# Kernel tuning notes

Measured on AMD Instinct MI355X. Metric: run time of the kernel, lower is better.

Reference implementation:

```python
import jax, jax.numpy as jnp
import numpy as np

NUM_QUBITS = 12
ENC_COPIES = 1
ANSATZ_COPIES = 2
BATCH = 1024
NUM_THETAS = NUM_QUBITS * (ANSATZ_COPIES + 1) * 2  # 72

_H = jnp.asarray(np.array([[1.0, 1.0], [1.0, -1.0]], np.complex64) / np.sqrt(2.0))


def _apply_1q(state, U, q):
    # state: [B, 2, 2, ..., 2] (n qubit axes); apply 2x2 unitary U on qubit q
    s = jnp.moveaxis(state, 1 + q, -1)
    s = jnp.einsum('...j,ij->...i', s, U)
    return jnp.moveaxis(s, -1, 1 + q)


def _apply_zpow(state, t, q):
    # cirq Z**t = diag(1, e^{i*pi*t}); t is scalar or per-batch [B]
    n = state.ndim - 1
    phase = jnp.exp(1j * jnp.pi * t).astype(jnp.complex64)
    factor = jnp.stack([jnp.ones_like(phase), phase], axis=-1)
    if factor.ndim == 2:  # batched exponent -> broadcast over other qubit axes
        factor = factor.reshape((factor.shape[0],) + (1,) * (n - 1) + (2,))
    s = jnp.moveaxis(state, 1 + q, -1)
    return jnp.moveaxis(s * factor, -1, 1 + q)


def _ypow_unitary(t):
    # cirq Y**t up to global phase e^{i*pi*t/2} (irrelevant for Z expectations)
    a = 0.5 * jnp.pi * t
    c, s = jnp.cos(a), jnp.sin(a)
    return jnp.stack([jnp.stack([c, -s]), jnp.stack([s, c])]).astype(jnp.complex64)


def _apply_cnot(state, c, t):
    s = jnp.moveaxis(state, (1 + c, 1 + t), (-2, -1))
    s = jnp.stack([s[..., 0, :], s[..., 1, ::-1]], axis=-2)
    return jnp.moveaxis(s, (-2, -1), (1 + c, 1 + t))


def _encoding_block(state, x):
    # FirstOrderPauliZEncoding: per copy, per qubit: H then Z**x_q
    for _ in range(ENC_COPIES):
        for q in range(NUM_QUBITS):
            state = _apply_1q(state, _H, q)
            state = _apply_zpow(state, x[:, q], q)
    return state


def _ansatz_block(state, th, with_cnot):
    # EfficientSU2 layer: Y**th[q,0], Z**th[q,1] per qubit, then CNOT chain
    for q in range(NUM_QUBITS):
        state = _apply_1q(state, _ypow_unitary(th[q, 0]), q)
        state = _apply_zpow(state, th[q, 1], q)
    if with_cnot:
        for q in range(NUM_QUBITS - 1):
            state = _apply_cnot(state, q, q + 1)
    return state


_enc = jax.checkpoint(_encoding_block)
_ans_cnot = jax.checkpoint(lambda st, th: _ansatz_block(st, th, True))
_ans_last = jax.checkpoint(lambda st, th: _ansatz_block(st, th, False))


def _circuit(inputs, thetas):
    b = inputs.shape[0]
    state = jnp.zeros((b, 2 ** NUM_QUBITS), jnp.complex64).at[:, 0].set(1.0)
    state = state.reshape((b,) + (2,) * NUM_QUBITS)
    state = _enc(state, inputs)
    th = thetas.reshape(ANSATZ_COPIES + 1, NUM_QUBITS, 2)
    for l in range(ANSATZ_COPIES + 1):
        state = (_ans_cnot if l < ANSATZ_COPIES else _ans_last)(state, th[l])
    # readouts: <Z_q> for each qubit
    probs = state.real ** 2 + state.imag ** 2
    exps = []
    for q in range(NUM_QUBITS):
        axes = tuple(a for a in range(1, NUM_QUBITS + 1) if a != 1 + q)
        p = probs.sum(axis=axes)  # [B, 2]
        exps.append(p[:, 0] - p[:, 1])
    return jnp.stack(exps, axis=-1)  # [B, NUM_QUBITS]


def setup_inputs() -> dict:
    key = jax.random.key(0)
    k1, k2 = jax.random.split(key)
    inputs = jax.random.uniform(k1, (BATCH, NUM_QUBITS), jnp.float32)
    thetas = jax.random.uniform(k2, (NUM_THETAS,), jnp.float32, minval=-1.0, maxval=1.0)
    return {"inputs": inputs, "thetas": thetas}


def reference(inputs, thetas):
    return _circuit(inputs, thetas)
```

## Files before the change

kernel.cpp:

```cpp
#include <hip/hip_runtime.h>


#define PI_F 3.14159265358979323846f
#define NR 32
#define PAD 66

typedef __attribute__((ext_vector_type(2))) float v2f;
typedef __attribute__((ext_vector_type(4))) float v4f;

__device__ __forceinline__ v2f mkv(float x, float y) { v2f r; r.x = x; r.y = y; return r; }
__device__ __forceinline__ v2f cmul(v2f a, v2f b) {
    return a.x * b + a.y * mkv(-b.y, b.x);
}
__device__ __forceinline__ v2f cmulc(v2f a, v2f b) {
    return a.x * mkv(b.x, -b.y) + a.y * mkv(b.y, b.x);
}

template<int M>
__device__ __forceinline__ float lane_xor_f(float v) {
    if constexpr (M == 1) {
        return __int_as_float(__builtin_amdgcn_update_dpp(
            0, __float_as_int(v), 0xB1, 0xF, 0xF, false));
    } else if constexpr (M == 2) {
        return __int_as_float(__builtin_amdgcn_update_dpp(
            0, __float_as_int(v), 0x4E, 0xF, 0xF, false));
    } else if constexpr (M == 4) {
        return __int_as_float(__builtin_amdgcn_ds_swizzle(__float_as_int(v), 0x101F));
    } else if constexpr (M == 8) {
        return __int_as_float(__builtin_amdgcn_ds_swizzle(__float_as_int(v), 0x201F));
    } else if constexpr (M == 16) {
        return __int_as_float(__builtin_amdgcn_ds_swizzle(__float_as_int(v), 0x401F));
    } else {
        return __shfl_xor(v, 32, 64);
    }
}

template<int RB>
__device__ __forceinline__ void ypow_reg(v2f (&a)[NR], float c, float s) {
    #pragma unroll
    for (int r0 = 0; r0 < NR; ++r0) {
        if ((r0 >> RB) & 1) continue;
        const int r1 = r0 | (1 << RB);
        v2f a0 = a[r0], a1 = a[r1];
        a[r0] = c * a0 - s * a1;
        a[r1] = s * a0 + c * a1;
    }
}

__device__ __forceinline__ void ypowA(v2f (&a)[NR], const v2f* __restrict__ yt) {
    { v2f t = yt[1]; ypow_reg<4>(a, t.x, t.y); }
    { v2f t = yt[2]; ypow_reg<3>(a, t.x, t.y); }
    { v2f t = yt[3]; ypow_reg<2>(a, t.x, t.y); }
    { v2f t = yt[4]; ypow_reg<1>(a, t.x, t.y); }
    { v2f t = yt[5]; ypow_reg<0>(a, t.x, t.y); }
}
__device__ __forceinline__ void ypowB(v2f (&a)[NR], const v2f* __restrict__ yt) {
    { v2f t = yt[7];  ypow_reg<4>(a, t.x, t.y); }
    { v2f t = yt[8];  ypow_reg<3>(a, t.x, t.y); }
    { v2f t = yt[9];  ypow_reg<2>(a, t.x, t.y); }
    { v2f t = yt[10]; ypow_reg<1>(a, t.x, t.y); }
    { v2f t = yt[11]; ypow_reg<0>(a, t.x, t.y); }
}

template<bool PRE_SYNC>
__device__ __forceinline__ void exchange_AB(v2f (&a)[NR], v2f* buf,
                                            int w, int lane, float c6, float s6) {
    v2f* wb = buf + w * (NR * PAD);
    if (PRE_SYNC) __syncthreads();
    #pragma unroll
    for (int r = 0; r < NR; ++r)
        wb[r * PAD + (lane & 31) * 2 + (lane >> 5)] = a[r];
    asm volatile("s_waitcnt lgkmcnt(0)" ::: "memory");
    const int g = lane >> 1;
    const float k0 = (lane & 1) ? s6 : c6;
    const float k1 = (lane & 1) ? c6 : -s6;
    #pragma unroll
    for (int r = 0; r < NR; ++r) {
        v4f p = *(const v4f*)(&wb[g * PAD + r * 2]);
        a[r] = k0 * p.xy + k1 * p.zw;
    }
}

__device__ __forceinline__ void exchange_BA(v2f (&a)[NR], v2f* buf,
                                            int w, int lane, float c0, float s0) {
    __syncthreads();
    const int p6w = lane ^ (w << 5);
    #pragma unroll
    for (int r = 0; r < NR; ++r)
        buf[p6w * PAD + r * 2 + w] = a[r];
    __syncthreads();
    const float k0 = w ? s0 : c0;
    const float k1 = w ? c0 : -s0;
    #pragma unroll
    for (int rp = 0; rp < NR; ++rp) {
        const int ylow = (rp << 6) | lane;
        const int t = ylow ^ (ylow >> 1);
        const int base = (t >> 5) * PAD + (t & 31) * 2;
        v4f p = *(const v4f*)(&buf[base]);
        a[rp] = k0 * p.xy + k1 * p.zw;
    }
}

__device__ __forceinline__ void fused_z_B(v2f (&a)[NR], int w, int lane,
                                          const float* __restrict__ th,
                                          const v2f* __restrict__ zt) {
    float alpha = w ? th[1] : 0.0f;
    #pragma unroll
    for (int k = 0; k < 6; ++k)
        alpha += ((lane >> k) & 1) ? th[2*(6-k)+1] : 0.0f;
    float zs, zc; __sincosf(PI_F * alpha, &zs, &zc);
    v2f zq[5];
    #pragma unroll
    for (int j = 0; j < 5; ++j) zq[j] = zt[j];
    const v2f base = mkv(zc, zs);
    v2f curs[4];
    curs[0] = base;
    curs[1] = cmul(base, cmul(zq[2], zq[3]));
    curs[2] = cmul(base, cmul(zq[3], zq[4]));
    curs[3] = cmul(base, cmul(zq[2], zq[4]));
    a[0]  = cmul(a[0],  curs[0]);
    a[12] = cmul(a[12], curs[1]);
    a[24] = cmul(a[24], curs[2]);
    a[20] = cmul(a[20], curs[3]);
    #pragma unroll
    for (int i = 1; i < 8; ++i) {
        #pragma unroll
        for (int m = 0; m < 4; ++m) {
            const int k = 8 * m + i;
            const int bit = __builtin_ctz(i);
            const int g = k ^ (k >> 1);
            curs[m] = ((g >> bit) & 1) ? cmul(curs[m], zq[bit])
                                       : cmulc(curs[m], zq[bit]);
            a[g] = cmul(a[g], curs[m]);
        }
    }
}

__global__ __launch_bounds__(128) void vqc_kernel(
    const float* __restrict__ inputs,
    const float* __restrict__ thetas,
    float* __restrict__ out)
{
    __shared__ __align__(16) v2f buf[64 * PAD];
    __shared__ v2f thTab[46];
    __shared__ float redBuf[24];

    const int b = blockIdx.x;
    const int tid = threadIdx.x;
    const int w = tid >> 6;
    const int lane = tid & 63;
    const float* x = inputs + b * 12;

    if (tid < 36) {
        const int l = tid / 12, q = tid % 12;
        float s, c; __sincosf(0.5f * PI_F * thetas[l * 24 + 2 * q], &s, &c);
        thTab[tid] = mkv(c, s);
    } else if (tid < 46) {
        const int j = tid - 36, l = j / 5, jj = j % 5;
        float s, c; __sincosf(PI_F * thetas[l * 24 + 2 * (11 - jj) + 1], &s, &c);
        thTab[tid] = mkv(c, s);
    }

    float phb = 0.0f;
    #pragma unroll
    for (int k = 0; k < 6; ++k)
        phb += ((lane >> k) & 1) ? x[11 - k] : 0.0f;
    float cbs, cbc; __sincosf(PI_F * phb, &cbs, &cbc);
    v2f cisb = mkv(cbc, cbs);
    float es, ec; __sincosf(PI_F * x[0], &es, &ec);
    v2f zr[5];
    #pragma unroll
    for (int j = 0; j < 5; ++j) {
        float ss, cc; __sincosf(PI_F * x[5 - j], &ss, &cc);
        zr[j] = mkv(cc, ss);
    }

    __syncthreads();

    v2f a[NR];
    {
        v2f t0 = thTab[0];
        v2f Fw = w ? mkv(t0.y + t0.x * ec,  t0.x * es)
                   : mkv(t0.x - t0.y * ec, -t0.y * es);
        const v2f g0 = cmul(Fw, cisb) * 0.015625f;
        v2f curs[4];
        curs[0] = g0;
        curs[1] = cmul(g0, cmul(zr[2], zr[3]));
        curs[2] = cmul(g0, cmul(zr[3], zr[4]));
        curs[3] = cmul(g0, cmul(zr[2], zr[4]));
        a[0] = curs[0]; a[12] = curs[1]; a[24] = curs[2]; a[20] = curs[3];
        #pragma unroll
        for (int i = 1; i < 8; ++i) {
            #pragma unroll
            for (int m = 0; m < 4; ++m) {
                const int k = 8 * m + i;
                const int bit = __builtin_ctz(i);
                const int g = k ^ (k >> 1);
                curs[m] = ((g >> bit) & 1) ? cmul(curs[m], zr[bit])
                                           : cmulc(curs[m], zr[bit]);
                a[g] = curs[m];
            }
        }
    }

    ypowA(a, &thTab[0]);
    { v2f t = thTab[6];  exchange_AB<false>(a, buf, w, lane, t.x, t.y); }
    ypowB(a, &thTab[0]);
    fused_z_B(a, w, lane, thetas, &thTab[36]);
    { v2f t = thTab[12]; exchange_BA(a, buf, w, lane, t.x, t.y); }

    ypowA(a, &thTab[12]);
    { v2f t = thTab[18]; exchange_AB<true>(a, buf, w, lane, t.x, t.y); }
    ypowB(a, &thTab[12]);
    fused_z_B(a, w, lane, thetas + 24, &thTab[41]);
    { v2f t = thTab[24]; exchange_BA(a, buf, w, lane, t.x, t.y); }

    ypowA(a, &thTab[24]);
    { v2f t = thTab[30]; exchange_AB<true>(a, buf, w, lane, t.x, t.y); }
    ypowB(a, &thTab[24]);

    float totalP = 0.0f;
    float D[5] = {0, 0, 0, 0, 0};
    #pragma unroll
    for (int r = 0; r < NR; ++r) {
        const float p = a[r].x * a[r].x + a[r].y * a[r].y;
        totalP += p;
        #pragma unroll
        for (int j = 0; j < 5; ++j)
            D[j] += ((r >> j) & 1) ? -p : p;
    }
    {
        float T = totalP;
        T += lane_xor_f<32>(T);
        T += lane_xor_f<16>(T);
        T += lane_xor_f<8>(T);
        T += lane_xor_f<4>(T);
        T += lane_xor_f<2>(T);
        T += lane_xor_f<1>(T);
        if (lane == 0) redBuf[w * 12 + 0] = w ? -T : T;
    }
    #pragma unroll
    for (int q = 1; q < 12; ++q) {
        float v;
        if (q <= 6)  v = ((lane >> (6 - q)) & 1) ? -totalP : totalP;
        else         v = D[11 - q];
        v += lane_xor_f<32>(v);
        v += lane_xor_f<16>(v);
        v += lane_xor_f<8>(v);
        v += lane_xor_f<4>(v);
        v += lane_xor_f<2>(v);
        v += lane_xor_f<1>(v);
        if (lane == 0) redBuf[w * 12 + q] = v;
    }
    __syncthreads();
    if (tid < 12) out[b * 12 + tid] = redBuf[tid] + redBuf[12 + tid];
}

extern "C" void kernel_launch(void* const* d_in, const int* in_sizes, int n_in,
                              void* d_out, int out_size, void* d_ws, size_t ws_size,
                              hipStream_t stream) {
    const float* inputs = (const float*)d_in[0];
    const float* thetas = (const float*)d_in[1];
    float* out = (float*)d_out;
    vqc_kernel<<<dim3(1024), dim3(128), 0, stream>>>(inputs, thetas, out);
}
```

Before: 74.61 us.

## Process two batch samples per block to amortize setup and increase ILP

Each block now simulates two circuits (two batch rows) at once, holding two 32-element register state arrays and interleaving their gate arithmetic, with the grid halved to 512 blocks. The shared theta-table setup and per-block overhead are amortized over two samples, and the interleaved independent chains give the scheduler more instruction-level parallelism. In exchange, register pressure roughly doubles, which may lower occupancy or cause spills. The LDS exchanges are serialized per sample with extra barriers, and fewer blocks are launched across the CUs.

```diff
diff --git a/kernel.cpp b/kernel.cpp
--- a/kernel.cpp
+++ b/kernel.cpp
@@ -36,74 +36,107 @@
 }
 
 template<int RB>
-__device__ __forceinline__ void ypow_reg(v2f (&a)[NR], float c, float s) {
+__device__ __forceinline__ void ypow_reg2(v2f (&aA)[NR], v2f (&aB)[NR],
+                                          float c, float s) {
     #pragma unroll
     for (int r0 = 0; r0 < NR; ++r0) {
         if ((r0 >> RB) & 1) continue;
         const int r1 = r0 | (1 << RB);
-        v2f a0 = a[r0], a1 = a[r1];
-        a[r0] = c * a0 - s * a1;
-        a[r1] = s * a0 + c * a1;
-    }
-}
-
-__device__ __forceinline__ void ypowA(v2f (&a)[NR], const v2f* __restrict__ yt) {
-    { v2f t = yt[1]; ypow_reg<4>(a, t.x, t.y); }
-    { v2f t = yt[2]; ypow_reg<3>(a, t.x, t.y); }
-    { v2f t = yt[3]; ypow_reg<2>(a, t.x, t.y); }
-    { v2f t = yt[4]; ypow_reg<1>(a, t.x, t.y); }
-    { v2f t = yt[5]; ypow_reg<0>(a, t.x, t.y); }
-}
-__device__ __forceinline__ void ypowB(v2f (&a)[NR], const v2f* __restrict__ yt) {
-    { v2f t = yt[7];  ypow_reg<4>(a, t.x, t.y); }
-    { v2f t = yt[8];  ypow_reg<3>(a, t.x, t.y); }
-    { v2f t = yt[9];  ypow_reg<2>(a, t.x, t.y); }
-    { v2f t = yt[10]; ypow_reg<1>(a, t.x, t.y); }
-    { v2f t = yt[11]; ypow_reg<0>(a, t.x, t.y); }
+        v2f A0 = aA[r0], A1 = aA[r1];
+        v2f B0 = aB[r0], B1 = aB[r1];
+        aA[r0] = c * A0 - s * A1;
+        aA[r1] = s * A0 + c * A1;
+        aB[r0] = c * B0 - s * B1;
+        aB[r1] = s * B0 + c * B1;
+    }
+}
+
+__device__ __forceinline__ void ypowA2(v2f (&aA)[NR], v2f (&aB)[NR],
+                                       const v2f* __restrict__ yt) {
+    { v2f t = yt[1]; ypow_reg2<4>(aA, aB, t.x, t.y); }
+    { v2f t = yt[2]; ypow_reg2<3>(aA, aB, t.x, t.y); }
+    { v2f t = yt[3]; ypow_reg2<2>(aA, aB, t.x, t.y); }
+    { v2f t = yt[4]; ypow_reg2<1>(aA, aB, t.x, t.y); }
+    { v2f t = yt[5]; ypow_reg2<0>(aA, aB, t.x, t.y); }
+}
+__device__ __forceinline__ void ypowB2(v2f (&aA)[NR], v2f (&aB)[NR],
+                                       const v2f* __restrict__ yt) {
+    { v2f t = yt[7];  ypow_reg2<4>(aA, aB, t.x, t.y); }
+    { v2f t = yt[8];  ypow_reg2<3>(aA, aB, t.x, t.y); }
+    { v2f t = yt[9];  ypow_reg2<2>(aA, aB, t.x, t.y); }
+    { v2f t = yt[10]; ypow_reg2<1>(aA, aB, t.x, t.y); }
+    { v2f t = yt[11]; ypow_reg2<0>(aA, aB, t.x, t.y); }
 }
 
 template<bool PRE_SYNC>
-__device__ __forceinline__ void exchange_AB(v2f (&a)[NR], v2f* buf,
-                                            int w, int lane, float c6, float s6) {
+__device__ __forceinline__ void exchange_AB2(v2f (&aA)[NR], v2f (&aB)[NR],
+                                             v2f* buf, int w, int lane,
+                                             float c6, float s6) {
     v2f* wb = buf + w * (NR * PAD);
     if (PRE_SYNC) __syncthreads();
-    #pragma unroll
-    for (int r = 0; r < NR; ++r)
-        wb[r * PAD + (lane & 31) * 2 + (lane >> 5)] = a[r];
-    asm volatile("s_waitcnt lgkmcnt(0)" ::: "memory");
+    const int wslot = (lane & 31) * 2 + (lane >> 5);
     const int g = lane >> 1;
     const float k0 = (lane & 1) ? s6 : c6;
     const float k1 = (lane & 1) ? c6 : -s6;
     #pragma unroll
+    for (int r = 0; r < NR; ++r)
+        wb[r * PAD + wslot] = aA[r];
+    asm volatile("s_waitcnt lgkmcnt(0)" ::: "memory");
+    #pragma unroll
     for (int r = 0; r < NR; ++r) {
         v4f p = *(const v4f*)(&wb[g * PAD + r * 2]);
-        a[r] = k0 * p.xy + k1 * p.zw;
-    }
-}
-
-__device__ __forceinline__ void exchange_BA(v2f (&a)[NR], v2f* buf,
-                                            int w, int lane, float c0, float s0) {
-    __syncthreads();
+        aA[r] = k0 * p.xy + k1 * p.zw;
+    }
+    asm volatile("" ::: "memory");
+    #pragma unroll
+    for (int r = 0; r < NR; ++r)
+        wb[r * PAD + wslot] = aB[r];
+    asm volatile("s_waitcnt lgkmcnt(0)" ::: "memory");
+    #pragma unroll
+    for (int r = 0; r < NR; ++r) {
+        v4f p = *(const v4f*)(&wb[g * PAD + r * 2]);
+        aB[r] = k0 * p.xy + k1 * p.zw;
+    }
+}
+
+__device__ __forceinline__ void exchange_BA2(v2f (&aA)[NR], v2f (&aB)[NR],
+                                             v2f* buf, int w, int lane,
+                                             float c0, float s0) {
     const int p6w = lane ^ (w << 5);
-    #pragma unroll
-    for (int r = 0; r < NR; ++r)
-        buf[p6w * PAD + r * 2 + w] = a[r];
-    __syncthreads();
     const float k0 = w ? s0 : c0;
     const float k1 = w ? c0 : -s0;
+    __syncthreads();
+    #pragma unroll
+    for (int r = 0; r < NR; ++r)
+        buf[p6w * PAD + r * 2 + w] = aA[r];
+    __syncthreads();
     #pragma unroll
     for (int rp = 0; rp < NR; ++rp) {
         const int ylow = (rp << 6) | lane;
         const int t = ylow ^ (ylow >> 1);
         const int base = (t >> 5) * PAD + (t & 31) * 2;
         v4f p = *(const v4f*)(&buf[base]);
-        a[rp] = k0 * p.xy + k1 * p.zw;
-    }
-}
-
-__device__ __forceinline__ void fused_z_B(v2f (&a)[NR], int w, int lane,
-                                          const float* __restrict__ th,
-                                          const v2f* __restrict__ zt) {
+        aA[rp] = k0 * p.xy + k1 * p.zw;
+    }
+    __syncthreads();
+    #pragma unroll
+    for (int r = 0; r < NR; ++r)
+        buf[p6w * PAD + r * 2 + w] = aB[r];
+    __syncthreads();
+    #pragma unroll
+    for (int rp = 0; rp < NR; ++rp) {
+        const int ylow = (rp << 6) | lane;
+        const int t = ylow ^ (ylow >> 1);
+        const int base = (t >> 5) * PAD + (t & 31) * 2;
+        v4f p = *(const v4f*)(&buf[base]);
+        aB[rp] = k0 * p.xy + k1 * p.zw;
+    }
+}
+
+__device__ __forceinline__ void fused_z2(v2f (&aA)[NR], v2f (&aB)[NR],
+                                         int w, int lane,
+                                         const float* __restrict__ th,
+                                         const v2f* __restrict__ zt) {
     float alpha = w ? th[1] : 0.0f;
     #pragma unroll
     for (int k = 0; k < 6; ++k)
@@ -118,10 +151,10 @@
     curs[1] = cmul(base, cmul(zq[2], zq[3]));
     curs[2] = cmul(base, cmul(zq[3], zq[4]));
     curs[3] = cmul(base, cmul(zq[2], zq[4]));
-    a[0]  = cmul(a[0],  curs[0]);
-    a[12] = cmul(a[12], curs[1]);
-    a[24] = cmul(a[24], curs[2]);
-    a[20] = cmul(a[20], curs[3]);
+    aA[0]  = cmul(aA[0],  curs[0]); aB[0]  = cmul(aB[0],  curs[0]);
+    aA[12] = cmul(aA[12], curs[1]); aB[12] = cmul(aB[12], curs[1]);
+    aA[24] = cmul(aA[24], curs[2]); aB[24] = cmul(aB[24], curs[2]);
+    aA[20] = cmul(aA[20], curs[3]); aB[20] = cmul(aB[20], curs[3]);
     #pragma unroll
     for (int i = 1; i < 8; ++i) {
         #pragma unroll
@@ -131,7 +164,8 @@
             const int g = k ^ (k >> 1);
             curs[m] = ((g >> bit) & 1) ? cmul(curs[m], zq[bit])
                                        : cmulc(curs[m], zq[bit]);
-            a[g] = cmul(a[g], curs[m]);
+            aA[g] = cmul(aA[g], curs[m]);
+            aB[g] = cmul(aB[g], curs[m]);
         }
     }
 }
@@ -143,13 +177,14 @@
 {
     __shared__ __align__(16) v2f buf[64 * PAD];
     __shared__ v2f thTab[46];
-    __shared__ float redBuf[24];
+    __shared__ float redBuf[2][24];
 
     const int b = blockIdx.x;
     const int tid = threadIdx.x;
     const int w = tid >> 6;
     const int lane = tid & 63;
-    const float* x = inputs + b * 12;
+    const float* xA = inputs + (2 * b) * 12;
+    const float* xB = inputs + (2 * b + 1) * 12;
 
     if (tid < 36) {
         const int l = tid / 12, q = tid % 12;
@@ -161,34 +196,43 @@
         thTab[tid] = mkv(c, s);
     }
 
-    float phb = 0.0f;
-    #pragma unroll
-    for (int k = 0; k < 6; ++k)
-        phb += ((lane >> k) & 1) ? x[11 - k] : 0.0f;
-    float cbs, cbc; __sincosf(PI_F * phb, &cbs, &cbc);
-    v2f cisb = mkv(cbc, cbs);
-    float es, ec; __sincosf(PI_F * x[0], &es, &ec);
-    v2f zr[5];
+    float phbA = 0.0f, phbB = 0.0f;
+    #pragma unroll
+    for (int k = 0; k < 6; ++k) {
+        const bool s = (lane >> k) & 1;
+        phbA += s ? xA[11 - k] : 0.0f;
+        phbB += s ? xB[11 - k] : 0.0f;
+    }
+    float cAs, cAc; __sincosf(PI_F * phbA, &cAs, &cAc);
+    float cBs, cBc; __sincosf(PI_F * phbB, &cBs, &cBc);
+    float eAs, eAc; __sincosf(PI_F * xA[0], &eAs, &eAc);
+    float eBs, eBc; __sincosf(PI_F * xB[0], &eBs, &eBc);
+    v2f zrA[5], zrB[5];
     #pragma unroll
     for (int j = 0; j < 5; ++j) {
-        float ss, cc; __sincosf(PI_F * x[5 - j], &ss, &cc);
-        zr[j] = mkv(cc, ss);
-    }
-
-    __syncthreads();
-
-    v2f a[NR];
+        float ss, cc;
+        __sincosf(PI_F * xA[5 - j], &ss, &cc); zrA[j] = mkv(cc, ss);
+        __sincosf(PI_F * xB[5 - j], &ss, &cc); zrB[j] = mkv(cc, ss);
+    }
+
+    __syncthreads();
+
+    v2f aA[NR], aB[NR];
     {
         v2f t0 = thTab[0];
-        v2f Fw = w ? mkv(t0.y + t0.x * ec,  t0.x * es)
-                   : mkv(t0.x - t0.y * ec, -t0.y * es);
-        const v2f g0 = cmul(Fw, cisb) * 0.015625f;
-        v2f curs[4];
-        curs[0] = g0;
-        curs[1] = cmul(g0, cmul(zr[2], zr[3]));
-        curs[2] = cmul(g0, cmul(zr[3], zr[4]));
-        curs[3] = cmul(g0, cmul(zr[2], zr[4]));
-        a[0] = curs[0]; a[12] = curs[1]; a[24] = curs[2]; a[20] = curs[3];
+        v2f FwA = w ? mkv(t0.y + t0.x * eAc,  t0.x * eAs)
+                    : mkv(t0.x - t0.y * eAc, -t0.y * eAs);
+        v2f FwB = w ? mkv(t0.y + t0.x * eBc,  t0.x * eBs)
+                    : mkv(t0.x - t0.y * eBc, -t0.y * eBs);
+        const v2f gA = cmul(FwA, mkv(cAc, cAs)) * 0.015625f;
+        const v2f gB = cmul(FwB, mkv(cBc, cBs)) * 0.015625f;
+        v2f cA[4], cB[4];
+        cA[0] = gA;                              cB[0] = gB;
+        cA[1] = cmul(gA, cmul(zrA[2], zrA[3]));  cB[1] = cmul(gB, cmul(zrB[2], zrB[3]));
+        cA[2] = cmul(gA, cmul(zrA[3], zrA[4]));  cB[2] = cmul(gB, cmul(zrB[3], zrB[4]));
+        cA[3] = cmul(gA, cmul(zrA[2], zrA[4]));  cB[3] = cmul(gB, cmul(zrB[2], zrB[4]));
+        aA[0] = cA[0]; aA[12] = cA[1]; aA[24] = cA[2]; aA[20] = cA[3];
+        aB[0] = cB[0]; aB[12] = cB[1]; aB[24] = cB[2]; aB[20] = cB[3];
         #pragma unroll
         for (int i = 1; i < 8; ++i) {
             #pragma unroll
@@ -196,64 +240,85 @@
                 const int k = 8 * m + i;
                 const int bit = __builtin_ctz(i);
                 const int g = k ^ (k >> 1);
-                curs[m] = ((g >> bit) & 1) ? cmul(curs[m], zr[bit])
-                                           : cmulc(curs[m], zr[bit]);
-                a[g] = curs[m];
+                cA[m] = ((g >> bit) & 1) ? cmul(cA[m], zrA[bit])
+                                         : cmulc(cA[m], zrA[bit]);
+                cB[m] = ((g >> bit) & 1) ? cmul(cB[m], zrB[bit])
+                                         : cmulc(cB[m], zrB[bit]);
+                aA[g] = cA[m];
+                aB[g] = cB[m];
             }
         }
     }
 
-    ypowA(a, &thTab[0]);
-    { v2f t = thTab[6];  exchange_AB<false>(a, buf, w, lane, t.x, t.y); }
-    ypowB(a, &thTab[0]);
-    fused_z_B(a, w, lane, thetas, &thTab[36]);
-    { v2f t = thTab[12]; exchange_BA(a, buf, w, lane, t.x, t.y); }
-
-    ypowA(a, &thTab[12]);
-    { v2f t = thTab[18]; exchange_AB<true>(a, buf, w, lane, t.x, t.y); }
-    ypowB(a, &thTab[12]);
-    fused_z_B(a, w, lane, thetas + 24, &thTab[41]);
-    { v2f t = thTab[24]; exchange_BA(a, buf, w, lane, t.x, t.y); }
-
-    ypowA(a, &thTab[24]);
-    { v2f t = thTab[30]; exchange_AB<true>(a, buf, w, lane, t.x, t.y); }
-    ypowB(a, &thTab[24]);
-
-    float totalP = 0.0f;
-    float D[5] = {0, 0, 0, 0, 0};
+    ypowA2(aA, aB, &thTab[0]);
+    { v2f t = thTab[6];  exchange_AB2<false>(aA, aB, buf, w, lane, t.x, t.y); }
+    ypowB2(aA, aB, &thTab[0]);
+    fused_z2(aA, aB, w, lane, thetas, &thTab[36]);
+    { v2f t = thTab[12]; exchange_BA2(aA, aB, buf, w, lane, t.x, t.y); }
+
+    ypowA2(aA, aB, &thTab[12]);
+    { v2f t = thTab[18]; exchange_AB2<true>(aA, aB, buf, w, lane, t.x, t.y); }
+    ypowB2(aA, aB, &thTab[12]);
+    fused_z2(aA, aB, w, lane, thetas + 24, &thTab[41]);
+    { v2f t = thTab[24]; exchange_BA2(aA, aB, buf, w, lane, t.x, t.y); }
+
+    ypowA2(aA, aB, &thTab[24]);
+    { v2f t = thTab[30]; exchange_AB2<true>(aA, aB, buf, w, lane, t.x, t.y); }
+    ypowB2(aA, aB, &thTab[24]);
+
+    float tpA = 0.0f, tpB = 0.0f;
+    float DA[5] = {0,0,0,0,0}, DB[5] = {0,0,0,0,0};
     #pragma unroll
     for (int r = 0; r < NR; ++r) {
-        const float p = a[r].x * a[r].x + a[r].y * a[r].y;
-        totalP += p;
+        const float pA = aA[r].x * aA[r].x + aA[r].y * aA[r].y;
+        const float pB = aB[r].x * aB[r].x + aB[r].y * aB[r].y;
+        tpA += pA; tpB += pB;
         #pragma unroll
-        for (int j = 0; j < 5; ++j)
-            D[j] += ((r >> j) & 1) ? -p : p;
+        for (int j = 0; j < 5; ++j) {
+            DA[j] += ((r >> j) & 1) ? -pA : pA;
+            DB[j] += ((r >> j) & 1) ? -pB : pB;
+        }
     }
     {
-        float T = totalP;
-        T += lane_xor_f<32>(T);
-        T += lane_xor_f<16>(T);
-        T += lane_xor_f<8>(T);
-        T += lane_xor_f<4>(T);
-        T += lane_xor_f<2>(T);
-        T += lane_xor_f<1>(T);
-        if (lane == 0) redBuf[w * 12 + 0] = w ? -T : T;
+        float TA = tpA, TB = tpB;
+        TA += lane_xor_f<32>(TA); TB += lane_xor_f<32>(TB);
+        TA += lane_xor_f<16>(TA); TB += lane_xor_f<16>(TB);
+        TA += lane_xor_f<8>(TA);  TB += lane_xor_f<8>(TB);
+        TA += lane_xor_f<4>(TA);  TB += lane_xor_f<4>(TB);
+        TA += lane_xor_f<2>(TA);  TB += lane_xor_f<2>(TB);
+        TA += lane_xor_f<1>(TA);  TB += lane_xor_f<1>(TB);
+        if (lane == 0) {
+            redBuf[0][w * 12 + 0] = w ? -TA : TA;
+            redBuf[1][w * 12 + 0] = w ? -TB : TB;
+        }
     }
     #pragma unroll
     for (int q = 1; q < 12; ++q) {
-        float v;
-        if (q <= 6)  v = ((lane >> (6 - q)) & 1) ? -totalP : totalP;
-        else         v = D[11 - q];
-        v += lane_xor_f<32>(v);
-        v += lane_xor_f<16>(v);
-        v += lane_xor_f<8>(v);
-        v += lane_xor_f<4>(v);
-        v += lane_xor_f<2>(v);
-        v += lane_xor_f<1>(v);
-        if (lane == 0) redBuf[w * 12 + q] = v;
-    }
-    __syncthreads();
-    if (tid < 12) out[b * 12 + tid] = redBuf[tid] + redBuf[12 + tid];
+        float vA, vB;
+        if (q <= 6) {
+            const bool s = (lane >> (6 - q)) & 1;
+            vA = s ? -tpA : tpA;
+            vB = s ? -tpB : tpB;
+        } else {
+            vA = DA[11 - q];
+            vB = DB[11 - q];
+        }
+        vA += lane_xor_f<32>(vA); vB += lane_xor_f<32>(vB);
+        vA += lane_xor_f<16>(vA); vB += lane_xor_f<16>(vB);
+        vA += lane_xor_f<8>(vA);  vB += lane_xor_f<8>(vB);
+        vA += lane_xor_f<4>(vA);  vB += lane_xor_f<4>(vB);
+        vA += lane_xor_f<2>(vA);  vB += lane_xor_f<2>(vB);
+        vA += lane_xor_f<1>(vA);  vB += lane_xor_f<1>(vB);
+        if (lane == 0) {
+            redBuf[0][w * 12 + q] = vA;
+            redBuf[1][w * 12 + q] = vB;
+        }
+    }
+    __syncthreads();
+    if (tid < 24) {
+        const int s = tid / 12, q = tid % 12;
+        out[(2 * b + s) * 12 + q] = redBuf[s][q] + redBuf[s][12 + q];
+    }
 }
 
 extern "C" void kernel_launch(void* const* d_in, const int* in_sizes, int n_in,
@@ -262,5 +327,5 @@
     const float* inputs = (const float*)d_in[0];
     const float* thetas = (const float*)d_in[1];
     float* out = (float*)d_out;
-    vqc_kernel<<<dim3(1024), dim3(128), 0, stream>>>(inputs, thetas, out);
-}
+    vqc_kernel<<<dim3(512), dim3(128), 0, stream>>>(inputs, thetas, out);
+}
```

Result: slower. 78.02 us (+4.6%).

## Simulate each circuit with one wavefront holding 64 amplitudes per lane

Applied to the files above, without the earlier changes.

Switches from two wavefronts per batch element (32 amplitudes per lane) to a single 64-lane wavefront holding 64 amplitudes per lane. All block barriers and the cross-wave reduction buffer go away, and qubit-axis transposes become wave-local LDS exchanges. The gray-code Z-phase pass is extended to eight starting points. The cost is doubled register pressure (128 floats of state per lane), which lowers occupancy and risks spills, and half as many threads are launched.

```diff
diff --git a/kernel.cpp b/kernel.cpp
--- a/kernel.cpp
+++ b/kernel.cpp
@@ -2,7 +2,7 @@
 
 
 #define PI_F 3.14159265358979323846f
-#define NR 32
+#define NR 64
 #define PAD 66
 
 typedef __attribute__((ext_vector_type(2))) float v2f;
@@ -36,7 +36,8 @@
 }
 
 template<int RB>
-__device__ __forceinline__ void ypow_reg(v2f (&a)[NR], float c, float s) {
+__device__ __forceinline__ void ypow_reg(v2f (&a)[NR], v2f cs) {
+    const float c = cs.x, s = cs.y;
     #pragma unroll
     for (int r0 = 0; r0 < NR; ++r0) {
         if ((r0 >> RB) & 1) continue;
@@ -48,151 +49,116 @@
 }
 
 __device__ __forceinline__ void ypowA(v2f (&a)[NR], const v2f* __restrict__ yt) {
-    { v2f t = yt[1]; ypow_reg<4>(a, t.x, t.y); }
-    { v2f t = yt[2]; ypow_reg<3>(a, t.x, t.y); }
-    { v2f t = yt[3]; ypow_reg<2>(a, t.x, t.y); }
-    { v2f t = yt[4]; ypow_reg<1>(a, t.x, t.y); }
-    { v2f t = yt[5]; ypow_reg<0>(a, t.x, t.y); }
+    ypow_reg<5>(a, yt[0]);
+    ypow_reg<4>(a, yt[1]);
+    ypow_reg<3>(a, yt[2]);
+    ypow_reg<2>(a, yt[3]);
+    ypow_reg<1>(a, yt[4]);
+    ypow_reg<0>(a, yt[5]);
 }
 __device__ __forceinline__ void ypowB(v2f (&a)[NR], const v2f* __restrict__ yt) {
-    { v2f t = yt[7];  ypow_reg<4>(a, t.x, t.y); }
-    { v2f t = yt[8];  ypow_reg<3>(a, t.x, t.y); }
-    { v2f t = yt[9];  ypow_reg<2>(a, t.x, t.y); }
-    { v2f t = yt[10]; ypow_reg<1>(a, t.x, t.y); }
-    { v2f t = yt[11]; ypow_reg<0>(a, t.x, t.y); }
-}
-
-template<bool PRE_SYNC>
-__device__ __forceinline__ void exchange_AB(v2f (&a)[NR], v2f* buf,
-                                            int w, int lane, float c6, float s6) {
-    v2f* wb = buf + w * (NR * PAD);
-    if (PRE_SYNC) __syncthreads();
+    ypow_reg<5>(a, yt[6]);
+    ypow_reg<4>(a, yt[7]);
+    ypow_reg<3>(a, yt[8]);
+    ypow_reg<2>(a, yt[9]);
+    ypow_reg<1>(a, yt[10]);
+    ypow_reg<0>(a, yt[11]);
+}
+
+__device__ __forceinline__ void exchange_AB(v2f (&a)[NR], v2f* buf, int lane) {
     #pragma unroll
     for (int r = 0; r < NR; ++r)
-        wb[r * PAD + (lane & 31) * 2 + (lane >> 5)] = a[r];
+        buf[r * PAD + lane] = a[r];
     asm volatile("s_waitcnt lgkmcnt(0)" ::: "memory");
-    const int g = lane >> 1;
-    const float k0 = (lane & 1) ? s6 : c6;
-    const float k1 = (lane & 1) ? c6 : -s6;
+    #pragma unroll
+    for (int r2 = 0; r2 < NR; r2 += 2) {
+        v4f p = *(const v4f*)(&buf[lane * PAD + r2]);
+        a[r2]     = p.xy;
+        a[r2 + 1] = p.zw;
+    }
+    asm volatile("" ::: "memory");
+}
+
+__device__ __forceinline__ void exchange_BA(v2f (&a)[NR], v2f* buf, int lane) {
+    int u = lane; u ^= u >> 1; u ^= u >> 2; u ^= u >> 4; u &= 63;
+    const int maskb = (u & 1) ? 63 : 0;
     #pragma unroll
     for (int r = 0; r < NR; ++r) {
-        v4f p = *(const v4f*)(&wb[g * PAD + r * 2]);
-        a[r] = k0 * p.xy + k1 * p.zw;
-    }
-}
-
-__device__ __forceinline__ void exchange_BA(v2f (&a)[NR], v2f* buf,
-                                            int w, int lane, float c0, float s0) {
-    __syncthreads();
-    const int p6w = lane ^ (w << 5);
-    #pragma unroll
-    for (int r = 0; r < NR; ++r)
-        buf[p6w * PAD + r * 2 + w] = a[r];
-    __syncthreads();
-    const float k0 = w ? s0 : c0;
-    const float k1 = w ? c0 : -s0;
-    #pragma unroll
-    for (int rp = 0; rp < NR; ++rp) {
-        const int ylow = (rp << 6) | lane;
-        const int t = ylow ^ (ylow >> 1);
-        const int base = (t >> 5) * PAD + (t & 31) * 2;
-        v4f p = *(const v4f*)(&buf[base]);
-        a[rp] = k0 * p.xy + k1 * p.zw;
-    }
-}
-
-__device__ __forceinline__ void fused_z_B(v2f (&a)[NR], int w, int lane,
-                                          const float* __restrict__ th,
-                                          const v2f* __restrict__ zt) {
-    float alpha = w ? th[1] : 0.0f;
-    #pragma unroll
-    for (int k = 0; k < 6; ++k)
-        alpha += ((lane >> k) & 1) ? th[2*(6-k)+1] : 0.0f;
-    float zs, zc; __sincosf(PI_F * alpha, &zs, &zc);
-    v2f zq[5];
-    #pragma unroll
-    for (int j = 0; j < 5; ++j) zq[j] = zt[j];
-    const v2f base = mkv(zc, zs);
-    v2f curs[4];
+        int pr = r; pr ^= pr >> 1; pr ^= pr >> 2; pr ^= pr >> 4; pr &= 63;
+        buf[(pr ^ maskb) * PAD + u] = a[r];
+    }
+    asm volatile("s_waitcnt lgkmcnt(0)" ::: "memory");
+    #pragma unroll
+    for (int r2 = 0; r2 < NR; r2 += 2) {
+        v4f p = *(const v4f*)(&buf[lane * PAD + r2]);
+        a[r2]     = p.xy;
+        a[r2 + 1] = p.zw;
+    }
+    asm volatile("" ::: "memory");
+}
+
+__device__ __forceinline__ void gray_starts(const v2f (&z)[6], v2f base,
+                                            v2f (&curs)[8]) {
+    const v2f z23 = cmul(z[2], z[3]);
+    const v2f z45 = cmul(z[4], z[5]);
+    const v2f z34 = cmul(z[3], z[4]);
+    const v2f z24 = cmul(z[2], z[4]);
+    const v2f z35 = cmul(z[3], z[5]);
+    const v2f z25 = cmul(z[2], z[5]);
     curs[0] = base;
-    curs[1] = cmul(base, cmul(zq[2], zq[3]));
-    curs[2] = cmul(base, cmul(zq[3], zq[4]));
-    curs[3] = cmul(base, cmul(zq[2], zq[4]));
-    a[0]  = cmul(a[0],  curs[0]);
-    a[12] = cmul(a[12], curs[1]);
-    a[24] = cmul(a[24], curs[2]);
-    a[20] = cmul(a[20], curs[3]);
-    #pragma unroll
-    for (int i = 1; i < 8; ++i) {
-        #pragma unroll
-        for (int m = 0; m < 4; ++m) {
-            const int k = 8 * m + i;
-            const int bit = __builtin_ctz(i);
-            const int g = k ^ (k >> 1);
-            curs[m] = ((g >> bit) & 1) ? cmul(curs[m], zq[bit])
-                                       : cmulc(curs[m], zq[bit]);
-            a[g] = cmul(a[g], curs[m]);
-        }
-    }
-}
-
-__global__ __launch_bounds__(128) void vqc_kernel(
+    curs[1] = cmul(base, z23);
+    curs[2] = cmul(base, z34);
+    curs[3] = cmul(base, z24);
+    curs[4] = cmul(base, z45);
+    curs[5] = cmul(base, cmul(z23, z45));
+    curs[6] = cmul(base, z35);
+    curs[7] = cmul(base, z25);
+}
+
+__global__ __launch_bounds__(64) void vqc_kernel(
     const float* __restrict__ inputs,
     const float* __restrict__ thetas,
     float* __restrict__ out)
 {
-    __shared__ __align__(16) v2f buf[64 * PAD];
-    __shared__ v2f thTab[46];
-    __shared__ float redBuf[24];
+    __shared__ __align__(16) v2f buf[NR * PAD];
+    __shared__ v2f thTab[48];
 
     const int b = blockIdx.x;
-    const int tid = threadIdx.x;
-    const int w = tid >> 6;
-    const int lane = tid & 63;
+    const int lane = threadIdx.x;
     const float* x = inputs + b * 12;
 
-    if (tid < 36) {
-        const int l = tid / 12, q = tid % 12;
+    if (lane < 36) {
+        const int l = lane / 12, q = lane % 12;
         float s, c; __sincosf(0.5f * PI_F * thetas[l * 24 + 2 * q], &s, &c);
-        thTab[tid] = mkv(c, s);
-    } else if (tid < 46) {
-        const int j = tid - 36, l = j / 5, jj = j % 5;
+        thTab[lane] = mkv(c, s);
+    } else if (lane < 48) {
+        const int j = lane - 36, l = j / 6, jj = j % 6;
         float s, c; __sincosf(PI_F * thetas[l * 24 + 2 * (11 - jj) + 1], &s, &c);
-        thTab[tid] = mkv(c, s);
-    }
-
-    float phb = 0.0f;
+        thTab[lane] = mkv(c, s);
+    }
+
+    float phl = 0.0f;
     #pragma unroll
     for (int k = 0; k < 6; ++k)
-        phb += ((lane >> k) & 1) ? x[11 - k] : 0.0f;
-    float cbs, cbc; __sincosf(PI_F * phb, &cbs, &cbc);
-    v2f cisb = mkv(cbc, cbs);
-    float es, ec; __sincosf(PI_F * x[0], &es, &ec);
-    v2f zr[5];
-    #pragma unroll
-    for (int j = 0; j < 5; ++j) {
+        phl += ((lane >> k) & 1) ? x[11 - k] : 0.0f;
+    float ps, pc; __sincosf(PI_F * phl, &ps, &pc);
+    v2f zr[6];
+    #pragma unroll
+    for (int j = 0; j < 6; ++j) {
         float ss, cc; __sincosf(PI_F * x[5 - j], &ss, &cc);
         zr[j] = mkv(cc, ss);
     }
-
-    __syncthreads();
-
     v2f a[NR];
     {
-        v2f t0 = thTab[0];
-        v2f Fw = w ? mkv(t0.y + t0.x * ec,  t0.x * es)
-                   : mkv(t0.x - t0.y * ec, -t0.y * es);
-        const v2f g0 = cmul(Fw, cisb) * 0.015625f;
-        v2f curs[4];
-        curs[0] = g0;
-        curs[1] = cmul(g0, cmul(zr[2], zr[3]));
-        curs[2] = cmul(g0, cmul(zr[3], zr[4]));
-        curs[3] = cmul(g0, cmul(zr[2], zr[4]));
+        const v2f base = mkv(pc, ps) * 0.015625f;
+        v2f curs[8];
+        gray_starts(zr, base, curs);
         a[0] = curs[0]; a[12] = curs[1]; a[24] = curs[2]; a[20] = curs[3];
+        a[48] = curs[4]; a[60] = curs[5]; a[40] = curs[6]; a[36] = curs[7];
         #pragma unroll
         for (int i = 1; i < 8; ++i) {
             #pragma unroll
-            for (int m = 0; m < 4; ++m) {
+            for (int m = 0; m < 8; ++m) {
                 const int k = 8 * m + i;
                 const int bit = __builtin_ctz(i);
                 const int g = k ^ (k >> 1);
@@ -203,57 +169,70 @@
         }
     }
 
-    ypowA(a, &thTab[0]);
-    { v2f t = thTab[6];  exchange_AB<false>(a, buf, w, lane, t.x, t.y); }
-    ypowB(a, &thTab[0]);
-    fused_z_B(a, w, lane, thetas, &thTab[36]);
-    { v2f t = thTab[12]; exchange_BA(a, buf, w, lane, t.x, t.y); }
-
-    ypowA(a, &thTab[12]);
-    { v2f t = thTab[18]; exchange_AB<true>(a, buf, w, lane, t.x, t.y); }
-    ypowB(a, &thTab[12]);
-    fused_z_B(a, w, lane, thetas + 24, &thTab[41]);
-    { v2f t = thTab[24]; exchange_BA(a, buf, w, lane, t.x, t.y); }
-
-    ypowA(a, &thTab[24]);
-    { v2f t = thTab[30]; exchange_AB<true>(a, buf, w, lane, t.x, t.y); }
-    ypowB(a, &thTab[24]);
+    asm volatile("s_waitcnt lgkmcnt(0)" ::: "memory");
+
+    #pragma unroll
+    for (int l = 0; l < 3; ++l) {
+        const v2f* yt = &thTab[l * 12];
+        ypowA(a, yt);
+        exchange_AB(a, buf, lane);
+        ypowB(a, yt);
+        if (l < 2) {
+            float alpha = 0.0f;
+            #pragma unroll
+            for (int k = 0; k < 6; ++k)
+                alpha += ((lane >> k) & 1) ? thetas[l * 24 + 2 * (5 - k) + 1] : 0.0f;
+            float zs, zc; __sincosf(PI_F * alpha, &zs, &zc);
+            v2f zq[6];
+            #pragma unroll
+            for (int j = 0; j < 6; ++j) zq[j] = thTab[36 + l * 6 + j];
+            v2f curs[8];
+            gray_starts(zq, mkv(zc, zs), curs);
+            a[0]  = cmul(a[0],  curs[0]); a[12] = cmul(a[12], curs[1]);
+            a[24] = cmul(a[24], curs[2]); a[20] = cmul(a[20], curs[3]);
+            a[48] = cmul(a[48], curs[4]); a[60] = cmul(a[60], curs[5]);
+            a[40] = cmul(a[40], curs[6]); a[36] = cmul(a[36], curs[7]);
+            #pragma unroll
+            for (int i = 1; i < 8; ++i) {
+                #pragma unroll
+                for (int m = 0; m < 8; ++m) {
+                    const int k = 8 * m + i;
+                    const int bit = __builtin_ctz(i);
+                    const int g = k ^ (k >> 1);
+                    curs[m] = ((g >> bit) & 1) ? cmul(curs[m], zq[bit])
+                                               : cmulc(curs[m], zq[bit]);
+                    a[g] = cmul(a[g], curs[m]);
+                }
+            }
+            exchange_BA(a, buf, lane);
+        }
+    }
 
     float totalP = 0.0f;
-    float D[5] = {0, 0, 0, 0, 0};
+    float D[6] = {0, 0, 0, 0, 0, 0};
     #pragma unroll
     for (int r = 0; r < NR; ++r) {
         const float p = a[r].x * a[r].x + a[r].y * a[r].y;
         totalP += p;
         #pragma unroll
-        for (int j = 0; j < 5; ++j)
+        for (int j = 0; j < 6; ++j)
             D[j] += ((r >> j) & 1) ? -p : p;
     }
-    {
-        float T = totalP;
-        T += lane_xor_f<32>(T);
-        T += lane_xor_f<16>(T);
-        T += lane_xor_f<8>(T);
-        T += lane_xor_f<4>(T);
-        T += lane_xor_f<2>(T);
-        T += lane_xor_f<1>(T);
-        if (lane == 0) redBuf[w * 12 + 0] = w ? -T : T;
-    }
-    #pragma unroll
-    for (int q = 1; q < 12; ++q) {
+    float res = 0.0f;
+    #pragma unroll
+    for (int q = 0; q < 12; ++q) {
         float v;
-        if (q <= 6)  v = ((lane >> (6 - q)) & 1) ? -totalP : totalP;
-        else         v = D[11 - q];
+        if (q <= 5) v = ((lane >> (5 - q)) & 1) ? -totalP : totalP;
+        else        v = D[11 - q];
         v += lane_xor_f<32>(v);
         v += lane_xor_f<16>(v);
         v += lane_xor_f<8>(v);
         v += lane_xor_f<4>(v);
         v += lane_xor_f<2>(v);
         v += lane_xor_f<1>(v);
-        if (lane == 0) redBuf[w * 12 + q] = v;
-    }
-    __syncthreads();
-    if (tid < 12) out[b * 12 + tid] = redBuf[tid] + redBuf[12 + tid];
+        if (lane == q) res = v;
+    }
+    if (lane < 12) out[b * 12 + lane] = res;
 }
 
 extern "C" void kernel_launch(void* const* d_in, const int* in_sizes, int n_in,
@@ -262,5 +241,5 @@
     const float* inputs = (const float*)d_in[0];
     const float* thetas = (const float*)d_in[1];
     float* out = (float*)d_out;
-    vqc_kernel<<<dim3(1024), dim3(128), 0, stream>>>(inputs, thetas, out);
-}
+    vqc_kernel<<<dim3(1024), dim3(64), 0, stream>>>(inputs, thetas, out);
+}
```

Measured after the change: 74.89 us. About the same (+0.4%).
